# Optimization experiments

Measured on AMD Instinct MI355X. Metric: run time of the kernel, lower is better.

The kernel has to match this reference:

```python
import jax, jax.numpy as jnp
import numpy as np

B, T, H, N_IN, N_OUT = 256, 1024, 512, 64, 64


def setup_inputs() -> dict:
    key = jax.random.key(0)
    k_x, k_w, k_win, k_wout = jax.random.split(key, 4)
    # nn.Linear(in, out, bias=False) weight has shape [out, in]
    X = jax.random.normal(k_x, (B, T, N_IN), dtype=jnp.float32)
    h0 = jnp.zeros((B, H), dtype=jnp.float32)
    W = jax.random.normal(k_w, (H, H), dtype=jnp.float32) / np.sqrt(H)
    W_in = jax.random.normal(k_win, (H, N_IN), dtype=jnp.float32) / np.sqrt(N_IN)
    W_out = jax.random.normal(k_wout, (N_OUT, H), dtype=jnp.float32) / np.sqrt(H)
    return {"X": X, "h0": h0, "W": W, "W_in": W_in, "W_out": W_out}


def reference(X, h0, W, W_in, W_out):
    # Precompute input projections for all timesteps in one big GEMM:
    # inp[b, t, h] = X[b, t, :] @ W_in.T  (same math as per-step W_in(x_t))
    inp = jnp.einsum("bti,hi->tbh", X, W_in)  # [T, B, H]

    def step(h, inp_t):
        h_next = jnp.tanh(h) @ W.T + inp_t  # [B, H]
        return h_next, h_next

    _, hidden = jax.lax.scan(step, h0, inp)  # hidden: [T, B, H]
    hidden = jnp.transpose(hidden, (1, 0, 2))  # [B, T, H]
    out = jnp.einsum("bth,oh->bto", hidden, W_out)  # [B, T, n_out]
    return out, hidden
```

## Files before the change

kernel.cpp:

```cpp
#include <hip/hip_runtime.h>
#include <stdint.h>

#define B_    256
#define T_    1024
#define H_    512
#define NIN_  64
#define NOUT_ 64

#define SC_NW   8
#define BBLK    4
#define HROW    528
#define KB_REG  11

typedef __attribute__((ext_vector_type(8))) short bf16x8;
typedef __attribute__((ext_vector_type(4))) float f32x4;

__device__ __forceinline__ short f2bf(float f) {
  uint32_t u = __float_as_uint(f);
  uint32_t r = (u + 0x7FFFu + ((u >> 16) & 1u)) >> 16;
  return (short)(r & 0xFFFFu);
}

__device__ __forceinline__ bf16x8 pack8(float4 lo, float4 hi) {
  bf16x8 s;
  s[0] = f2bf(lo.x); s[1] = f2bf(lo.y); s[2] = f2bf(lo.z); s[3] = f2bf(lo.w);
  s[4] = f2bf(hi.x); s[5] = f2bf(hi.y); s[6] = f2bf(hi.z); s[7] = f2bf(hi.w);
  return s;
}

__device__ __forceinline__ float fast_tanh(float x) {
  float e = __expf(2.0f * x);
  return 1.0f - __fdividef(2.0f, e + 1.0f);
}

__global__ __launch_bounds__(512) void wprep(
    const float* __restrict__ W, short* __restrict__ sw)
{
  const int c = blockIdx.x * 512 + threadIdx.x;
  if (c >= 8 * 12 * 64) return;
  const int l  = c & 63;
  const int su = (c >> 6) % 12;
  const int w  = c / (12 * 64);
  const int kb = 13 + (su >> 2);
  const int jt = su & 3;
  const int col = 64 * w + 16 * jt + (l & 15);
  const int k0  = 32 * kb + (l >> 4) * 8;
  const float4* p = reinterpret_cast<const float4*>(W + (size_t)col * H_ + k0);
  *reinterpret_cast<bf16x8*>(sw + (size_t)c * 8) = pack8(p[0], p[1]);
}

#define XP_BLOCKS 512
__global__ __launch_bounds__(512, 2) void xproj(
    const float* __restrict__ X, const float* __restrict__ Win,
    float* __restrict__ inp)
{
  const int tid  = threadIdx.x;
  const int lane = tid & 63;
  const int w    = tid >> 6;
  const int g    = lane >> 4;
  const int m    = lane & 15;

  bf16x8 Bf[2][4];
#pragma unroll
  for (int kb = 0; kb < 2; ++kb)
#pragma unroll
    for (int jt = 0; jt < 4; ++jt) {
      const int j = 64 * w + 16 * jt + m;
      const float4* p = reinterpret_cast<const float4*>(Win + (size_t)j * NIN_ + 32 * kb + 8 * g);
      Bf[kb][jt] = pack8(p[0], p[1]);
    }

  const int NTILES = (B_ * T_) / 16;
  const f32x4 zero = {0.f, 0.f, 0.f, 0.f};

  for (int tile = blockIdx.x; tile < NTILES; tile += XP_BLOCKS) {
    const size_t row0 = (size_t)tile * 16;
    f32x4 acc[4];
    {
      const float4* p = reinterpret_cast<const float4*>(X + (row0 + m) * NIN_ + 8 * g);
      const bf16x8 a = pack8(p[0], p[1]);
#pragma unroll
      for (int jt = 0; jt < 4; ++jt)
        acc[jt] = __builtin_amdgcn_mfma_f32_16x16x32_bf16(a, Bf[0][jt], zero, 0, 0, 0);
    }
    {
      const float4* p = reinterpret_cast<const float4*>(X + (row0 + m) * NIN_ + 32 + 8 * g);
      const bf16x8 a = pack8(p[0], p[1]);
#pragma unroll
      for (int jt = 0; jt < 4; ++jt)
        acc[jt] = __builtin_amdgcn_mfma_f32_16x16x32_bf16(a, Bf[1][jt], acc[jt], 0, 0, 0);
    }
#pragma unroll
    for (int jt = 0; jt < 4; ++jt)
#pragma unroll
      for (int r = 0; r < 4; ++r)
        inp[(row0 + 4 * g + r) * H_ + 64 * w + 16 * jt + m] = acc[jt][r];
  }
}

__global__ __launch_bounds__(SC_NW * 64, 2) void rnn_scan(
    const float* __restrict__ h0, const float* __restrict__ W,
    float* __restrict__ hid, const short* __restrict__ swbuf)
{
  __shared__ __align__(16) short wlds[SC_NW * 8 * 64 * 8];
  __shared__ __align__(16) short hbuf[2][BBLK][HROW];

  const int tid  = threadIdx.x;
  const int lane = tid & 63;
  const int w    = tid >> 6;
  const int g    = lane >> 4;
  const int m    = lane & 15;
  const int b0   = blockIdx.x * BBLK;

  bf16x8 Wf[KB_REG * 4];
#pragma unroll
  for (int kb = 0; kb < KB_REG; ++kb)
#pragma unroll
    for (int jt = 0; jt < 4; ++jt) {
      const int j = 64 * w + 16 * jt + m;
      const float4* p = reinterpret_cast<const float4*>(W + (size_t)j * H_ + 32 * kb + 8 * g);
      Wf[kb * 4 + jt] = pack8(p[0], p[1]);
    }

#pragma unroll
  for (int i = 0; i < 8; ++i) {
    const int c  = tid + 512 * i;
    const int l  = c & 63;
    const int u  = (c >> 6) & 7;
    const int ww = c >> 9;
    const int kb = KB_REG + (u >> 2);
    const int jt = u & 3;
    const int col = 64 * ww + 16 * jt + (l & 15);
    const int k0  = 32 * kb + (l >> 4) * 8;
    const float4* p = reinterpret_cast<const float4*>(W + (size_t)col * H_ + k0);
    *reinterpret_cast<bf16x8*>(&wlds[((size_t)(ww * 8 + u) * 64 + l) * 8]) = pack8(p[0], p[1]);
  }

  for (int e = tid; e < BBLK * H_; e += SC_NW * 64) {
    const int r = e >> 9, k = e & (H_ - 1);
    hbuf[0][r][k] = f2bf(fast_tanh(h0[(size_t)(b0 + r) * H_ + k]));
  }

  const bf16x8* SW = reinterpret_cast<const bf16x8*>(swbuf);
  const int sbase = w * 12 * 64 + lane;
  bf16x8 Xb0 = SW[sbase + 0 * 64], Xb1 = SW[sbase + 1 * 64],
         Xb2 = SW[sbase + 2 * 64], Xb3 = SW[sbase + 3 * 64];
  bf16x8 Yb0 = SW[sbase + 4 * 64], Yb1 = SW[sbase + 5 * 64],
         Yb2 = SW[sbase + 6 * 64], Yb3 = SW[sbase + 7 * 64];

  float inp_cur[4];
#pragma unroll
  for (int r = 0; r < 4; ++r)
    inp_cur[r] = hid[((size_t)(b0 + r) * T_ + 0) * H_ + 64 * w + lane];

  __syncthreads();

  const f32x4 zero = {0.f, 0.f, 0.f, 0.f};
  const int arow = m & 3;

#pragma clang loop unroll(disable)
  for (int t = 0; t < T_; ++t) {
    const int cur = t & 1, nxt = cur ^ 1;
    const short* hr = &hbuf[cur][arow][0];

    f32x4 acc[4];

    {
      const bf16x8 a = *reinterpret_cast<const bf16x8*>(hr + 32 * 13 + 8 * g);
      acc[0] = __builtin_amdgcn_mfma_f32_16x16x32_bf16(a, Xb0, zero, 0, 0, 0);
      acc[1] = __builtin_amdgcn_mfma_f32_16x16x32_bf16(a, Xb1, zero, 0, 0, 0);
      acc[2] = __builtin_amdgcn_mfma_f32_16x16x32_bf16(a, Xb2, zero, 0, 0, 0);
      acc[3] = __builtin_amdgcn_mfma_f32_16x16x32_bf16(a, Xb3, zero, 0, 0, 0);
    }
    Xb0 = SW[sbase + 8 * 64];  Xb1 = SW[sbase + 9 * 64];
    Xb2 = SW[sbase + 10 * 64]; Xb3 = SW[sbase + 11 * 64];

    float inp_nxt[4];
    if (t + 1 < T_) {
#pragma unroll
      for (int r = 0; r < 4; ++r)
        inp_nxt[r] = hid[((size_t)(b0 + r) * T_ + (t + 1)) * H_ + 64 * w + lane];
    }

#pragma unroll
    for (int kb = 0; kb < KB_REG; ++kb) {
      const bf16x8 a = *reinterpret_cast<const bf16x8*>(hr + 32 * kb + 8 * g);
      acc[0] = __builtin_amdgcn_mfma_f32_16x16x32_bf16(a, Wf[kb * 4 + 0], acc[0], 0, 0, 0);
      acc[1] = __builtin_amdgcn_mfma_f32_16x16x32_bf16(a, Wf[kb * 4 + 1], acc[1], 0, 0, 0);
      acc[2] = __builtin_amdgcn_mfma_f32_16x16x32_bf16(a, Wf[kb * 4 + 2], acc[2], 0, 0, 0);
      acc[3] = __builtin_amdgcn_mfma_f32_16x16x32_bf16(a, Wf[kb * 4 + 3], acc[3], 0, 0, 0);
    }

#pragma unroll
    for (int kk = 0; kk < 2; ++kk) {
      const int kb = KB_REG + kk;
      const bf16x8 a = *reinterpret_cast<const bf16x8*>(hr + 32 * kb + 8 * g);
#pragma unroll
      for (int jt = 0; jt < 4; ++jt) {
        const bf16x8 b = *reinterpret_cast<const bf16x8*>(
            &wlds[((size_t)(w * 8 + kk * 4 + jt) * 64 + lane) * 8]);
        acc[jt] = __builtin_amdgcn_mfma_f32_16x16x32_bf16(a, b, acc[jt], 0, 0, 0);
      }
    }

    {
      const bf16x8 a = *reinterpret_cast<const bf16x8*>(hr + 32 * 14 + 8 * g);
      acc[0] = __builtin_amdgcn_mfma_f32_16x16x32_bf16(a, Yb0, acc[0], 0, 0, 0);
      acc[1] = __builtin_amdgcn_mfma_f32_16x16x32_bf16(a, Yb1, acc[1], 0, 0, 0);
      acc[2] = __builtin_amdgcn_mfma_f32_16x16x32_bf16(a, Yb2, acc[2], 0, 0, 0);
      acc[3] = __builtin_amdgcn_mfma_f32_16x16x32_bf16(a, Yb3, acc[3], 0, 0, 0);
    }
    Yb0 = SW[sbase + 4 * 64]; Yb1 = SW[sbase + 5 * 64];
    Yb2 = SW[sbase + 6 * 64]; Yb3 = SW[sbase + 7 * 64];

    {
      const bf16x8 a = *reinterpret_cast<const bf16x8*>(hr + 32 * 15 + 8 * g);
      acc[0] = __builtin_amdgcn_mfma_f32_16x16x32_bf16(a, Xb0, acc[0], 0, 0, 0);
      acc[1] = __builtin_amdgcn_mfma_f32_16x16x32_bf16(a, Xb1, acc[1], 0, 0, 0);
      acc[2] = __builtin_amdgcn_mfma_f32_16x16x32_bf16(a, Xb2, acc[2], 0, 0, 0);
      acc[3] = __builtin_amdgcn_mfma_f32_16x16x32_bf16(a, Xb3, acc[3], 0, 0, 0);
    }
    Xb0 = SW[sbase + 0 * 64]; Xb1 = SW[sbase + 1 * 64];
    Xb2 = SW[sbase + 2 * 64]; Xb3 = SW[sbase + 3 * 64];

#pragma unroll
    for (int r = 0; r < 4; ++r) {
      float v = acc[0][r];
      v = (g == 1) ? acc[1][r] : v;
      v = (g == 2) ? acc[2][r] : v;
      v = (g == 3) ? acc[3][r] : v;
      v += inp_cur[r];
      hid[((size_t)(b0 + r) * T_ + t) * H_ + 64 * w + lane] = v;
      hbuf[nxt][r][64 * w + lane] = f2bf(fast_tanh(v));
    }
#pragma unroll
    for (int r = 0; r < 4; ++r) inp_cur[r] = inp_nxt[r];

    asm volatile("s_waitcnt lgkmcnt(0)" ::: "memory");
    __builtin_amdgcn_s_barrier();
    asm volatile("" ::: "memory");
  }
}

#define OP_BLOCKS 1024
#define OP_WAVES  8
__global__ __launch_bounds__(OP_WAVES * 64, 2) void out_proj(
    const float* __restrict__ hid, const float* __restrict__ Wout,
    float* __restrict__ out)
{
  __shared__ __align__(16) short ws[16][NOUT_][32];

  const int tid  = threadIdx.x;
  const int lane = tid & 63;
  const int w    = tid >> 6;
  const int g    = lane >> 4;
  const int m    = lane & 15;

#pragma unroll
  for (int i = 0; i < 8; ++i) {
    const int c   = tid + OP_WAVES * 64 * i;
    const int kb  = c >> 8;
    const int col = (c >> 2) & 63;
    const int q   = (c & 3) * 8;
    const float4* p = reinterpret_cast<const float4*>(Wout + (size_t)col * H_ + 32 * kb + q);
    *reinterpret_cast<bf16x8*>(&ws[kb][col][q]) = pack8(p[0], p[1]);
  }
  __syncthreads();

  const int wave_id = blockIdx.x * OP_WAVES + w;
  const int NWAVES  = OP_BLOCKS * OP_WAVES;
  const int NTILES  = (B_ * T_) / 16;

  for (int tile = wave_id; tile < NTILES; tile += NWAVES) {
    const size_t row0 = (size_t)tile * 16;
    f32x4 acc[4];
    {
      const float4* p = reinterpret_cast<const float4*>(hid + (row0 + m) * H_ + 8 * g);
      const bf16x8 a = pack8(p[0], p[1]);
      const f32x4 zero = {0.f, 0.f, 0.f, 0.f};
#pragma unroll
      for (int jt = 0; jt < 4; ++jt) {
        const bf16x8 b = *reinterpret_cast<const bf16x8*>(&ws[0][16 * jt + m][8 * g]);
        acc[jt] = __builtin_amdgcn_mfma_f32_16x16x32_bf16(a, b, zero, 0, 0, 0);
      }
    }
#pragma unroll
    for (int kb = 1; kb < 16; ++kb) {
      const float4* p = reinterpret_cast<const float4*>(hid + (row0 + m) * H_ + 32 * kb + 8 * g);
      const bf16x8 a = pack8(p[0], p[1]);
#pragma unroll
      for (int jt = 0; jt < 4; ++jt) {
        const bf16x8 b = *reinterpret_cast<const bf16x8*>(&ws[kb][16 * jt + m][8 * g]);
        acc[jt] = __builtin_amdgcn_mfma_f32_16x16x32_bf16(a, b, acc[jt], 0, 0, 0);
      }
    }
#pragma unroll
    for (int jt = 0; jt < 4; ++jt)
#pragma unroll
      for (int r = 0; r < 4; ++r)
        out[(row0 + 4 * g + r) * NOUT_ + 16 * jt + m] = acc[jt][r];
  }
}

extern "C" void kernel_launch(void* const* d_in, const int* in_sizes, int n_in,
                              void* d_out, int out_size, void* d_ws, size_t ws_size,
                              hipStream_t stream) {
  const float* X    = (const float*)d_in[0];
  const float* h0   = (const float*)d_in[1];
  const float* W    = (const float*)d_in[2];
  const float* Win  = (const float*)d_in[3];
  const float* Wout = (const float*)d_in[4];

  float* out = (float*)d_out;
  float* hid = (float*)d_out + (size_t)B_ * T_ * NOUT_;
  short* sw  = (short*)d_out;

  wprep<<<dim3(12), dim3(512), 0, stream>>>(W, sw);
  xproj<<<dim3(XP_BLOCKS), dim3(512), 0, stream>>>(X, Win, hid);
  rnn_scan<<<dim3(B_ / BBLK), dim3(SC_NW * 64), 0, stream>>>(h0, W, hid, sw);
  out_proj<<<dim3(OP_BLOCKS), dim3(OP_WAVES * 64), 0, stream>>>(hid, Wout, out);
}
```

Baseline: 2.919 ms.

## Stream six W k-blocks from global via double buffer, drop LDS weight tiles

```diff
diff --git a/kernel.cpp b/kernel.cpp
--- a/kernel.cpp
+++ b/kernel.cpp
@@ -10,7 +10,9 @@
 #define SC_NW   8
 #define BBLK    4
 #define HROW    528
-#define KB_REG  11
+#define KB_REG  10
+#define KB_STR  6
+#define SW_CHUNKS (SC_NW * KB_STR * 4 * 64)
 
 typedef __attribute__((ext_vector_type(8))) short bf16x8;
 typedef __attribute__((ext_vector_type(4))) float f32x4;
@@ -37,14 +39,15 @@
     const float* __restrict__ W, short* __restrict__ sw)
 {
   const int c = blockIdx.x * 512 + threadIdx.x;
-  if (c >= 8 * 12 * 64) return;
-  const int l  = c & 63;
-  const int su = (c >> 6) % 12;
-  const int w  = c / (12 * 64);
-  const int kb = 13 + (su >> 2);
-  const int jt = su & 3;
-  const int col = 64 * w + 16 * jt + (l & 15);
-  const int k0  = 32 * kb + (l >> 4) * 8;
+  if (c >= SW_CHUNKS) return;
+  const int lane = c & 63;
+  const int u    = c >> 6;
+  const int jt   = u & 3;
+  const int gw   = u >> 2;
+  const int G    = gw % KB_STR;
+  const int w    = gw / KB_STR;
+  const int col  = 64 * w + 16 * jt + (lane & 15);
+  const int k0   = 32 * (KB_REG + G) + (lane >> 4) * 8;
   const float4* p = reinterpret_cast<const float4*>(W + (size_t)col * H_ + k0);
   *reinterpret_cast<bf16x8*>(sw + (size_t)c * 8) = pack8(p[0], p[1]);
 }
@@ -98,11 +101,12 @@
   }
 }
 
-__global__ __launch_bounds__(SC_NW * 64, 2) void rnn_scan(
+__global__
+__attribute__((amdgpu_flat_work_group_size(512, 512), amdgpu_waves_per_eu(2, 2)))
+void rnn_scan(
     const float* __restrict__ h0, const float* __restrict__ W,
     float* __restrict__ hid, const short* __restrict__ swbuf)
 {
-  __shared__ __align__(16) short wlds[SC_NW * 8 * 64 * 8];
   __shared__ __align__(16) short hbuf[2][BBLK][HROW];
 
   const int tid  = threadIdx.x;
@@ -112,116 +116,100 @@
   const int m    = lane & 15;
   const int b0   = blockIdx.x * BBLK;
 
-  bf16x8 Wf[KB_REG * 4];
+  bf16x8 Wf[KB_REG][4];
 #pragma unroll
   for (int kb = 0; kb < KB_REG; ++kb)
 #pragma unroll
     for (int jt = 0; jt < 4; ++jt) {
-      const int j = 64 * w + 16 * jt + m;
-      const float4* p = reinterpret_cast<const float4*>(W + (size_t)j * H_ + 32 * kb + 8 * g);
-      Wf[kb * 4 + jt] = pack8(p[0], p[1]);
-    }
-
-#pragma unroll
-  for (int i = 0; i < 8; ++i) {
-    const int c  = tid + 512 * i;
-    const int l  = c & 63;
-    const int u  = (c >> 6) & 7;
-    const int ww = c >> 9;
-    const int kb = KB_REG + (u >> 2);
-    const int jt = u & 3;
-    const int col = 64 * ww + 16 * jt + (l & 15);
-    const int k0  = 32 * kb + (l >> 4) * 8;
-    const float4* p = reinterpret_cast<const float4*>(W + (size_t)col * H_ + k0);
-    *reinterpret_cast<bf16x8*>(&wlds[((size_t)(ww * 8 + u) * 64 + l) * 8]) = pack8(p[0], p[1]);
-  }
+      const int col = 64 * w + 16 * jt + m;
+      const float4* p = reinterpret_cast<const float4*>(W + (size_t)col * H_ + 32 * kb + 8 * g);
+      Wf[kb][jt] = pack8(p[0], p[1]);
+    }
 
   for (int e = tid; e < BBLK * H_; e += SC_NW * 64) {
     const int r = e >> 9, k = e & (H_ - 1);
     hbuf[0][r][k] = f2bf(fast_tanh(h0[(size_t)(b0 + r) * H_ + k]));
   }
 
+  const int mycol = 64 * w + 16 * g + m;
+  float inp_cur[4];
+#pragma unroll
+  for (int r = 0; r < 4; ++r)
+    inp_cur[r] = hid[((size_t)(b0 + r) * T_ + 0) * H_ + mycol];
+
+  const int sbase = (w * KB_STR * 4) * 64 + lane;
   const bf16x8* SW = reinterpret_cast<const bf16x8*>(swbuf);
-  const int sbase = w * 12 * 64 + lane;
-  bf16x8 Xb0 = SW[sbase + 0 * 64], Xb1 = SW[sbase + 1 * 64],
-         Xb2 = SW[sbase + 2 * 64], Xb3 = SW[sbase + 3 * 64];
-  bf16x8 Yb0 = SW[sbase + 4 * 64], Yb1 = SW[sbase + 5 * 64],
-         Yb2 = SW[sbase + 6 * 64], Yb3 = SW[sbase + 7 * 64];
-
-  float inp_cur[4];
-#pragma unroll
-  for (int r = 0; r < 4; ++r)
-    inp_cur[r] = hid[((size_t)(b0 + r) * T_ + 0) * H_ + 64 * w + lane];
+  bf16x8 s0[4], s1[4];
+#pragma unroll
+  for (int jt = 0; jt < 4; ++jt) s0[jt] = SW[sbase + (0 * 4 + jt) * 64];
+#pragma unroll
+  for (int jt = 0; jt < 4; ++jt) s1[jt] = SW[sbase + (1 * 4 + jt) * 64];
 
   __syncthreads();
-
-  const f32x4 zero = {0.f, 0.f, 0.f, 0.f};
-  const int arow = m & 3;
 
 #pragma clang loop unroll(disable)
   for (int t = 0; t < T_; ++t) {
     const int cur = t & 1, nxt = cur ^ 1;
-    const short* hr = &hbuf[cur][arow][0];
-
+
+    uintptr_t swo_u = (uintptr_t)SW;
+    asm volatile("" : "+s"(swo_u));
+    const bf16x8* SWo = (const bf16x8*)swo_u;
+
+    float inp_nxt[4] = {0.f, 0.f, 0.f, 0.f};
+    if (t + 1 < T_) {
+#pragma unroll
+      for (int r = 0; r < 4; ++r)
+        inp_nxt[r] = hid[((size_t)(b0 + r) * T_ + (t + 1)) * H_ + mycol];
+    }
+
+    const short* hr = &hbuf[cur][m & 3][0];
     f32x4 acc[4];
-
-    {
-      const bf16x8 a = *reinterpret_cast<const bf16x8*>(hr + 32 * 13 + 8 * g);
-      acc[0] = __builtin_amdgcn_mfma_f32_16x16x32_bf16(a, Xb0, zero, 0, 0, 0);
-      acc[1] = __builtin_amdgcn_mfma_f32_16x16x32_bf16(a, Xb1, zero, 0, 0, 0);
-      acc[2] = __builtin_amdgcn_mfma_f32_16x16x32_bf16(a, Xb2, zero, 0, 0, 0);
-      acc[3] = __builtin_amdgcn_mfma_f32_16x16x32_bf16(a, Xb3, zero, 0, 0, 0);
-    }
-    Xb0 = SW[sbase + 8 * 64];  Xb1 = SW[sbase + 9 * 64];
-    Xb2 = SW[sbase + 10 * 64]; Xb3 = SW[sbase + 11 * 64];
-
-    float inp_nxt[4];
-    if (t + 1 < T_) {
-#pragma unroll
-      for (int r = 0; r < 4; ++r)
-        inp_nxt[r] = hid[((size_t)(b0 + r) * T_ + (t + 1)) * H_ + 64 * w + lane];
-    }
-
-#pragma unroll
-    for (int kb = 0; kb < KB_REG; ++kb) {
-      const bf16x8 a = *reinterpret_cast<const bf16x8*>(hr + 32 * kb + 8 * g);
-      acc[0] = __builtin_amdgcn_mfma_f32_16x16x32_bf16(a, Wf[kb * 4 + 0], acc[0], 0, 0, 0);
-      acc[1] = __builtin_amdgcn_mfma_f32_16x16x32_bf16(a, Wf[kb * 4 + 1], acc[1], 0, 0, 0);
-      acc[2] = __builtin_amdgcn_mfma_f32_16x16x32_bf16(a, Wf[kb * 4 + 2], acc[2], 0, 0, 0);
-      acc[3] = __builtin_amdgcn_mfma_f32_16x16x32_bf16(a, Wf[kb * 4 + 3], acc[3], 0, 0, 0);
-    }
-
-#pragma unroll
-    for (int kk = 0; kk < 2; ++kk) {
-      const int kb = KB_REG + kk;
-      const bf16x8 a = *reinterpret_cast<const bf16x8*>(hr + 32 * kb + 8 * g);
-#pragma unroll
-      for (int jt = 0; jt < 4; ++jt) {
-        const bf16x8 b = *reinterpret_cast<const bf16x8*>(
-            &wlds[((size_t)(w * 8 + kk * 4 + jt) * 64 + lane) * 8]);
-        acc[jt] = __builtin_amdgcn_mfma_f32_16x16x32_bf16(a, b, acc[jt], 0, 0, 0);
+#pragma unroll
+    for (int jt = 0; jt < 4; ++jt) acc[jt] = (f32x4){0.f, 0.f, 0.f, 0.f};
+
+#pragma unroll
+    for (int ph = 0; ph < 5; ++ph) {
+#pragma unroll
+      for (int kk = 0; kk < 2; ++kk) {
+        const int kb = 2 * ph + kk;
+        const bf16x8 a = *reinterpret_cast<const bf16x8*>(hr + 32 * kb + 8 * g);
+#pragma unroll
+        for (int jt = 0; jt < 4; ++jt)
+          acc[jt] = __builtin_amdgcn_mfma_f32_16x16x32_bf16(a, Wf[kb][jt], acc[jt], 0, 0, 0);
       }
-    }
-
+      if (ph < 4) {
+        const bf16x8 a = *reinterpret_cast<const bf16x8*>(hr + 32 * (KB_REG + ph) + 8 * g);
+        if ((ph & 1) == 0) {
+#pragma unroll
+          for (int jt = 0; jt < 4; ++jt)
+            acc[jt] = __builtin_amdgcn_mfma_f32_16x16x32_bf16(a, s0[jt], acc[jt], 0, 0, 0);
+#pragma unroll
+          for (int jt = 0; jt < 4; ++jt) s0[jt] = SWo[sbase + ((ph + 2) * 4 + jt) * 64];
+        } else {
+#pragma unroll
+          for (int jt = 0; jt < 4; ++jt)
+            acc[jt] = __builtin_amdgcn_mfma_f32_16x16x32_bf16(a, s1[jt], acc[jt], 0, 0, 0);
+#pragma unroll
+          for (int jt = 0; jt < 4; ++jt) s1[jt] = SWo[sbase + ((ph + 2) * 4 + jt) * 64];
+        }
+      }
+    }
     {
       const bf16x8 a = *reinterpret_cast<const bf16x8*>(hr + 32 * 14 + 8 * g);
-      acc[0] = __builtin_amdgcn_mfma_f32_16x16x32_bf16(a, Yb0, acc[0], 0, 0, 0);
-      acc[1] = __builtin_amdgcn_mfma_f32_16x16x32_bf16(a, Yb1, acc[1], 0, 0, 0);
-      acc[2] = __builtin_amdgcn_mfma_f32_16x16x32_bf16(a, Yb2, acc[2], 0, 0, 0);
-      acc[3] = __builtin_amdgcn_mfma_f32_16x16x32_bf16(a, Yb3, acc[3], 0, 0, 0);
-    }
-    Yb0 = SW[sbase + 4 * 64]; Yb1 = SW[sbase + 5 * 64];
-    Yb2 = SW[sbase + 6 * 64]; Yb3 = SW[sbase + 7 * 64];
-
+#pragma unroll
+      for (int jt = 0; jt < 4; ++jt)
+        acc[jt] = __builtin_amdgcn_mfma_f32_16x16x32_bf16(a, s0[jt], acc[jt], 0, 0, 0);
+    }
     {
       const bf16x8 a = *reinterpret_cast<const bf16x8*>(hr + 32 * 15 + 8 * g);
-      acc[0] = __builtin_amdgcn_mfma_f32_16x16x32_bf16(a, Xb0, acc[0], 0, 0, 0);
-      acc[1] = __builtin_amdgcn_mfma_f32_16x16x32_bf16(a, Xb1, acc[1], 0, 0, 0);
-      acc[2] = __builtin_amdgcn_mfma_f32_16x16x32_bf16(a, Xb2, acc[2], 0, 0, 0);
-      acc[3] = __builtin_amdgcn_mfma_f32_16x16x32_bf16(a, Xb3, acc[3], 0, 0, 0);
-    }
-    Xb0 = SW[sbase + 0 * 64]; Xb1 = SW[sbase + 1 * 64];
-    Xb2 = SW[sbase + 2 * 64]; Xb3 = SW[sbase + 3 * 64];
+#pragma unroll
+      for (int jt = 0; jt < 4; ++jt)
+        acc[jt] = __builtin_amdgcn_mfma_f32_16x16x32_bf16(a, s1[jt], acc[jt], 0, 0, 0);
+    }
+#pragma unroll
+    for (int jt = 0; jt < 4; ++jt) s0[jt] = SWo[sbase + (0 * 4 + jt) * 64];
+#pragma unroll
+    for (int jt = 0; jt < 4; ++jt) s1[jt] = SWo[sbase + (1 * 4 + jt) * 64];
 
 #pragma unroll
     for (int r = 0; r < 4; ++r) {
@@ -230,8 +218,8 @@
       v = (g == 2) ? acc[2][r] : v;
       v = (g == 3) ? acc[3][r] : v;
       v += inp_cur[r];
-      hid[((size_t)(b0 + r) * T_ + t) * H_ + 64 * w + lane] = v;
-      hbuf[nxt][r][64 * w + lane] = f2bf(fast_tanh(v));
+      hid[((size_t)(b0 + r) * T_ + t) * H_ + mycol] = v;
+      hbuf[nxt][r][mycol] = f2bf(fast_tanh(v));
     }
 #pragma unroll
     for (int r = 0; r < 4; ++r) inp_cur[r] = inp_nxt[r];
@@ -313,9 +301,11 @@
 
   float* out = (float*)d_out;
   float* hid = (float*)d_out + (size_t)B_ * T_ * NOUT_;
-  short* sw  = (short*)d_out;
-
-  wprep<<<dim3(12), dim3(512), 0, stream>>>(W, sw);
+
+  const size_t out_elems = (size_t)B_ * T_ * NOUT_;
+  short* sw = (short*)((float*)d_out + out_elems) - (size_t)SW_CHUNKS * 8;
+
+  wprep<<<dim3(SW_CHUNKS / 512), dim3(512), 0, stream>>>(W, sw);
   xproj<<<dim3(XP_BLOCKS), dim3(512), 0, stream>>>(X, Win, hid);
   rnn_scan<<<dim3(B_ / BBLK), dim3(SC_NW * 64), 0, stream>>>(h0, W, hid, sw);
   out_proj<<<dim3(OP_BLOCKS), dim3(OP_WAVES * 64), 0, stream>>>(hid, Wout, out);
```

Result: no change. 2.925 ms (+0.2%).
